# Kernel tuning notes

Hardware: AMD Instinct MI355X
Metric: run time of the kernel (lower is better)

Reference implementation:

```python
import jax, jax.numpy as jnp
import numpy as np

H = 16
D_MODEL = 1024
D_K = D_MODEL // H  # 64


def setup_inputs() -> dict:
    key = jax.random.key(0)
    ks = jax.random.split(key, 8)
    B, S = 8, 1024
    q = jax.random.normal(ks[0], (B, S, D_MODEL), dtype=jnp.float32)
    k = jax.random.normal(ks[1], (B, S, D_MODEL), dtype=jnp.float32)
    v = jax.random.normal(ks[2], (B, S, D_MODEL), dtype=jnp.float32)
    # xavier_normal for [h, d_model, d_k]: std = sqrt(2 / (d_model + d_k)) (fan over last two dims)
    std_p = float(np.sqrt(2.0 / (D_MODEL + D_K)))
    W_q = jax.random.normal(ks[3], (H, D_MODEL, D_K), dtype=jnp.float32) * std_p
    W_k = jax.random.normal(ks[4], (H, D_MODEL, D_K), dtype=jnp.float32) * std_p
    W_v = jax.random.normal(ks[5], (H, D_MODEL, D_K), dtype=jnp.float32) * std_p
    std_o = float(np.sqrt(2.0 / (H * D_K + D_MODEL)))
    W_o = jax.random.normal(ks[6], (D_MODEL, H * D_K), dtype=jnp.float32) * std_o  # torch Linear weight [out, in]
    b_o = jax.random.normal(ks[7], (D_MODEL,), dtype=jnp.float32) * 0.01
    return {"q": q, "k": k, "v": v, "W_q": W_q, "W_k": W_k, "W_v": W_v, "W_o": W_o, "b_o": b_o}


def reference(q, k, v, W_q, W_k, W_v, W_o, b_o):
    B, S, _ = q.shape
    # per-head projections: [h, b, s, d_k]
    qh = jnp.einsum('bsd,hdk->hbsk', q, W_q)
    kh = jnp.einsum('bsd,hdk->hbsk', k, W_k)
    vh = jnp.einsum('bsd,hdk->hbsk', v, W_v)
    scale = 1.0 / jnp.sqrt(jnp.asarray(D_K, dtype=q.dtype))
    scores = jnp.einsum('hbsk,hbtk->hbst', qh, kh) * scale  # [h,b,s,s]
    attn = jax.nn.softmax(scores, axis=-1)
    c = jnp.einsum('hbst,hbtk->hbsk', attn, vh)  # [h,b,s,d_k]
    # torch code splits the stacked (h*b) batch and concats on feature dim:
    # head index becomes the OUTER factor of the feature dim -> [b,s,h*d_k]
    c = jnp.transpose(c, (1, 2, 0, 3)).reshape(B, S, H * D_K)
    out = c @ W_o.T + b_o
    return out
```

## Files before the change

### kernel.cpp

```cpp
#include <hip/hip_runtime.h>
#include <hip/hip_bf16.h>

typedef __bf16 bf16_t;
typedef __attribute__((ext_vector_type(8))) __bf16 bf16x8;
typedef __attribute__((ext_vector_type(4))) float f32x4;

#define MFMA(a, b, c) __builtin_amdgcn_mfma_f32_16x16x32_bf16(a, b, c, 0, 0, 0)

__device__ inline void gload_lds16(const bf16_t* g, bf16_t* l) {
  __builtin_amdgcn_global_load_lds(
      (const __attribute__((address_space(1))) void*)g,
      (__attribute__((address_space(3))) void*)l, 16, 0, 0);
}

__global__ void fill_sentinel(float* out, int n, float val) {
  int i = blockIdx.x * blockDim.x + threadIdx.x;
  if (i < n) out[i] = val;
}

__global__ void transpose_w(const float* __restrict__ Wq, const float* __restrict__ Wk,
                            const float* __restrict__ Wv, bf16_t* __restrict__ Wt) {
  int gid = blockIdx.x * blockDim.x + threadIdx.x;
  int e = gid * 8;
  int m = e >> 20;
  int rem = e & 1048575;
  int n = rem >> 10;
  int d0 = rem & 1023;
  const float* W = (m == 0) ? Wq : (m == 1) ? Wk : Wv;
  int h = n >> 6, kk = n & 63;
  union { bf16_t h8[8]; uint4 u; } tmp;
#pragma unroll
  for (int j = 0; j < 8; ++j)
    tmp.h8[j] = (bf16_t)W[((size_t)(h * 1024 + d0 + j)) * 64 + kk];
  *(uint4*)(Wt + e) = tmp.u;
}

__global__ void cvt_bf16(const float* __restrict__ in, bf16_t* __restrict__ out) {
  size_t i = (size_t)(blockIdx.x * blockDim.x + threadIdx.x) * 8;
  f32x4 a = *(const f32x4*)(in + i);
  f32x4 b = *(const f32x4*)(in + i + 4);
  bf16x8 r;
  r[0] = (bf16_t)a[0]; r[1] = (bf16_t)a[1]; r[2] = (bf16_t)a[2]; r[3] = (bf16_t)a[3];
  r[4] = (bf16_t)b[0]; r[5] = (bf16_t)b[1]; r[6] = (bf16_t)b[2]; r[7] = (bf16_t)b[3];
  *(bf16x8*)(out + i) = r;
}

template <int MODE>
__global__ void gemm_bt(const bf16_t* __restrict__ A, const bf16_t* __restrict__ Bt,
                        const float* __restrict__ bias, void* __restrict__ out_,
                        int M, int N, int K, float scale) {
  __shared__ bf16_t sA[128 * 32];
  __shared__ bf16_t sB[128 * 32];
  const int t = threadIdx.x;
  const int w = t >> 6, l = t & 63;
  const int lq = l >> 4, ll = l & 15;
  const int m0 = blockIdx.x * 128, n0 = blockIdx.y * 128;
  const int wr = (w >> 1) * 64, wc = (w & 1) * 64;
  const int srow = l >> 2;
  const int scol = (l & 3) * 8;
  f32x4 acc[4][4] = {};
  for (int k0 = 0; k0 < K; k0 += 32) {
    __syncthreads();
#pragma unroll
    for (int c = 0; c < 2; ++c) {
      int ch = w * 2 + c;
      int row = ch * 16 + srow;
      gload_lds16(A  + (size_t)(m0 + row) * K + k0 + scol, sA + ch * 512);
      gload_lds16(Bt + (size_t)(n0 + row) * K + k0 + scol, sB + ch * 512);
    }
    __syncthreads();
    bf16x8 af[4], bfr[4];
#pragma unroll
    for (int i = 0; i < 4; ++i) {
      af[i]  = *(const bf16x8*)(sA + (wr + i * 16 + ll) * 32 + lq * 8);
      bfr[i] = *(const bf16x8*)(sB + (wc + i * 16 + ll) * 32 + lq * 8);
    }
#pragma unroll
    for (int mi = 0; mi < 4; ++mi)
#pragma unroll
      for (int ni = 0; ni < 4; ++ni)
        acc[mi][ni] = MFMA(af[mi], bfr[ni], acc[mi][ni]);
  }
#pragma unroll
  for (int mi = 0; mi < 4; ++mi)
#pragma unroll
    for (int ni = 0; ni < 4; ++ni)
#pragma unroll
      for (int r = 0; r < 4; ++r) {
        int row = m0 + wr + mi * 16 + lq * 4 + r;
        int col = n0 + wc + ni * 16 + ll;
        float v = acc[mi][ni][r];
        if (MODE == 2) {
          ((float*)out_)[(size_t)row * N + col] = v + bias[col];
        } else {
          int h = col >> 6, kk = col & 63, b = row >> 10, s = row & 1023;
          size_t idx;
          if (MODE == 0)
            idx = ((size_t)((h * 8 + b) * 1024 + s)) * 64 + kk;
          else
            idx = ((size_t)((h * 8 + b) * 64 + kk)) * 1024 + s;
          ((bf16_t*)out_)[idx] = (bf16_t)(v * scale);
        }
      }
}

__global__ void attn_kernel(const bf16_t* __restrict__ qh, const bf16_t* __restrict__ kh,
                            const bf16_t* __restrict__ vt, bf16_t* __restrict__ c) {
  constexpr int QP = 72, KP = 72, PP = 72;
  __shared__ bf16_t sQ[64 * QP];
  __shared__ bf16_t sK[64 * KP];
  __shared__ bf16_t sP[4][16 * PP];
  const int t = threadIdx.x;
  const int w = t >> 6, l = t & 63;
  const int lq = l >> 4, ll = l & 15;
  const int orig = blockIdx.x + (blockIdx.y << 4);
  const int wg = (orig & 7) * 256 + (orig >> 3);
  const int q0 = (wg & 15) * 64;
  const int hb = wg >> 4;
  const int h = hb >> 3, b = hb & 7;
  const size_t base = (size_t)hb * 65536;
  const bf16_t* Q = qh + base + (size_t)q0 * 64;
  const bf16_t* K = kh + base;
  const bf16_t* V = vt + base;
#pragma unroll
  for (int r = 0; r < 2; ++r) {
    int e = (r * 256 + t) * 8;
    int row = e >> 6, col = e & 63;
    *(uint4*)(sQ + row * QP + col) = *(const uint4*)(Q + e);
  }
  float mrow[4], lrow[4];
  f32x4 o[4] = {};
#pragma unroll
  for (int r = 0; r < 4; ++r) { mrow[r] = -1e30f; lrow[r] = 0.f; }

  for (int kt = 0; kt < 1024; kt += 64) {
    __syncthreads();
#pragma unroll
    for (int r = 0; r < 2; ++r) {
      int e = (r * 256 + t) * 8;
      int row = e >> 6, col = e & 63;
      *(uint4*)(sK + row * KP + col) = *(const uint4*)(K + (size_t)kt * 64 + e);
    }
    __syncthreads();
    f32x4 sacc[4] = {};
    bf16x8 aq[2];
#pragma unroll
    for (int ks = 0; ks < 2; ++ks)
      aq[ks] = *(const bf16x8*)(sQ + (w * 16 + ll) * QP + ks * 32 + lq * 8);
#pragma unroll
    for (int ni = 0; ni < 4; ++ni)
#pragma unroll
      for (int ks = 0; ks < 2; ++ks) {
        bf16x8 bk = *(const bf16x8*)(sK + (ni * 16 + ll) * KP + ks * 32 + lq * 8);
        sacc[ni] = MFMA(aq[ks], bk, sacc[ni]);
      }
    float rmax[4] = {-1e30f, -1e30f, -1e30f, -1e30f};
#pragma unroll
    for (int ni = 0; ni < 4; ++ni)
#pragma unroll
      for (int r = 0; r < 4; ++r)
        rmax[r] = fmaxf(rmax[r], sacc[ni][r]);
    bool ok = true;
#pragma unroll
    for (int r = 0; r < 4; ++r)
      ok = ok && (rmax[r] <= mrow[r] + 8.0f);
    if (!__all(ok)) {
#pragma unroll
      for (int off = 1; off < 16; off <<= 1)
#pragma unroll
        for (int r = 0; r < 4; ++r)
          rmax[r] = fmaxf(rmax[r], __shfl_xor(rmax[r], off));
#pragma unroll
      for (int r = 0; r < 4; ++r) {
        float mnew = fmaxf(mrow[r], rmax[r]);
        float alpha = __expf(mrow[r] - mnew);
        mrow[r] = mnew;
        lrow[r] *= alpha;
#pragma unroll
        for (int ni = 0; ni < 4; ++ni)
          o[ni][r] *= alpha;
      }
    }
#pragma unroll
    for (int ni = 0; ni < 4; ++ni)
#pragma unroll
      for (int r = 0; r < 4; ++r) {
        float p = __expf(sacc[ni][r] - mrow[r]);
        sacc[ni][r] = p;
        lrow[r] += p;
      }
    bf16_t* Pw = sP[w];
#pragma unroll
    for (int ni = 0; ni < 4; ++ni)
#pragma unroll
      for (int r = 0; r < 4; ++r)
        Pw[(lq * 4 + r) * PP + ni * 16 + ll] = (bf16_t)sacc[ni][r];
    asm volatile("s_waitcnt lgkmcnt(0)" ::: "memory");
#pragma unroll
    for (int ks = 0; ks < 2; ++ks) {
      bf16x8 ap = *(const bf16x8*)(Pw + ll * PP + ks * 32 + lq * 8);
#pragma unroll
      for (int ni = 0; ni < 4; ++ni) {
        bf16x8 bv = *(const bf16x8*)(V + (size_t)(ni * 16 + ll) * 1024 + kt + ks * 32 + lq * 8);
        o[ni] = MFMA(ap, bv, o[ni]);
      }
    }
  }
#pragma unroll
  for (int off = 1; off < 16; off <<= 1)
#pragma unroll
    for (int r = 0; r < 4; ++r)
      lrow[r] += __shfl_xor(lrow[r], off);
#pragma unroll
  for (int ni = 0; ni < 4; ++ni)
#pragma unroll
    for (int r = 0; r < 4; ++r) {
      int s = q0 + w * 16 + lq * 4 + r;
      int dk = ni * 16 + ll;
      float val = o[ni][r] / lrow[r];
      c[((size_t)(b * 1024 + s)) * 1024 + h * 64 + dk] = (bf16_t)val;
    }
}

extern "C" void kernel_launch(void* const* d_in, const int* in_sizes, int n_in,
                              void* d_out, int out_size, void* d_ws, size_t ws_size,
                              hipStream_t stream) {
  float* out = (float*)d_out;
  int nblk_out = (out_size + 255) / 256;
  if (n_in != 8) {
    fill_sentinel<<<nblk_out, 256, 0, stream>>>(out, out_size, 600.0f + 10.0f * n_in);
    return;
  }
  const int expect[8] = {8388608, 8388608, 8388608, 1048576,
                         1048576, 1048576, 1048576, 1024};
  for (int i = 0; i < 8; ++i)
    if (in_sizes[i] != expect[i]) {
      fill_sentinel<<<nblk_out, 256, 0, stream>>>(out, out_size, 500.0f + 10.0f * i);
      return;
    }

  bf16_t* ws   = (bf16_t*)d_ws;
  bf16_t* qhb  = ws;
  bf16_t* khb  = ws + 8388608;
  bf16_t* vtb  = ws + 16777216;
  bf16_t* Wt   = ws + 25165824;
  bf16_t* cbuf = ws + 25165824;
  bf16_t* Wob  = ws;
  if (ws_size < 67108864ull) {
    fill_sentinel<<<nblk_out, 256, 0, stream>>>(out, out_size, 400.0f);
    return;
  }

  const float* q  = (const float*)d_in[0];
  const float* k  = (const float*)d_in[1];
  const float* v  = (const float*)d_in[2];
  const float* Wq = (const float*)d_in[3];
  const float* Wk = (const float*)d_in[4];
  const float* Wv = (const float*)d_in[5];
  const float* Wo = (const float*)d_in[6];
  const float* bo = (const float*)d_in[7];

  bf16_t* qb = (bf16_t*)d_out;
  bf16_t* kb = (bf16_t*)d_out + 8388608;
  bf16_t* vb = (bf16_t*)d_out;

  transpose_w<<<1536, 256, 0, stream>>>(Wq, Wk, Wv, Wt);
  cvt_bf16<<<4096, 256, 0, stream>>>(q, qb);
  cvt_bf16<<<4096, 256, 0, stream>>>(k, kb);
  dim3 gg(64, 8);
  gemm_bt<0><<<gg, 256, 0, stream>>>(qb, Wt,           nullptr, qhb, 8192, 1024, 1024, 0.125f);
  gemm_bt<0><<<gg, 256, 0, stream>>>(kb, Wt + 1048576, nullptr, khb, 8192, 1024, 1024, 1.0f);
  cvt_bf16<<<4096, 256, 0, stream>>>(v, vb);
  gemm_bt<1><<<gg, 256, 0, stream>>>(vb, Wt + 2097152, nullptr, vtb, 8192, 1024, 1024, 1.0f);
  attn_kernel<<<dim3(16, 128), 256, 0, stream>>>(qhb, khb, vtb, cbuf);
  cvt_bf16<<<512, 256, 0, stream>>>(Wo, Wob);
  gemm_bt<2><<<gg, 256, 0, stream>>>(cbuf, Wob, bo, out, 8192, 1024, 1024, 1.0f);
}
```

Before: 429.2 us.

## Double-buffer K tiles via registers and prefetch V in attention loop

The attention kernel now loads Q fragments straight into registers instead of staging them in shared memory. K tiles are double-buffered: the next tile is fetched into registers at the start of each iteration and written to the alternate LDS buffer at the end, so one barrier per iteration replaces two. V fragments are issued early, before the QK MFMAs, to hide global latency. The cost is higher register pressure, which may lower occupancy.

Result: slower. 451.9 us (+5.3%).

```diff
diff --git a/kernel.cpp b/kernel.cpp
--- a/kernel.cpp
+++ b/kernel.cpp
@@ -106,9 +106,8 @@
 
 __global__ void attn_kernel(const bf16_t* __restrict__ qh, const bf16_t* __restrict__ kh,
                             const bf16_t* __restrict__ vt, bf16_t* __restrict__ c) {
-  constexpr int QP = 72, KP = 72, PP = 72;
-  __shared__ bf16_t sQ[64 * QP];
-  __shared__ bf16_t sK[64 * KP];
+  constexpr int KP = 72, PP = 72;
+  __shared__ bf16_t sK[2][64 * KP];
   __shared__ bf16_t sP[4][16 * PP];
   const int t = threadIdx.x;
   const int w = t >> 6, l = t & 63;
@@ -122,36 +121,52 @@
   const bf16_t* Q = qh + base + (size_t)q0 * 64;
   const bf16_t* K = kh + base;
   const bf16_t* V = vt + base;
+
+  bf16x8 aq[2];
+#pragma unroll
+  for (int ks = 0; ks < 2; ++ks)
+    aq[ks] = *(const bf16x8*)(Q + (w * 16 + ll) * 64 + ks * 32 + lq * 8);
+
+  uint4 kreg[2];
+#pragma unroll
+  for (int r = 0; r < 2; ++r) {
+    int e = (r * 256 + t) * 8;
+    kreg[r] = *(const uint4*)(K + e);
+  }
 #pragma unroll
   for (int r = 0; r < 2; ++r) {
     int e = (r * 256 + t) * 8;
     int row = e >> 6, col = e & 63;
-    *(uint4*)(sQ + row * QP + col) = *(const uint4*)(Q + e);
-  }
+    *(uint4*)(sK[0] + row * KP + col) = kreg[r];
+  }
+  __syncthreads();
+
   float mrow[4], lrow[4];
   f32x4 o[4] = {};
 #pragma unroll
   for (int r = 0; r < 4; ++r) { mrow[r] = -1e30f; lrow[r] = 0.f; }
 
-  for (int kt = 0; kt < 1024; kt += 64) {
-    __syncthreads();
-#pragma unroll
-    for (int r = 0; r < 2; ++r) {
-      int e = (r * 256 + t) * 8;
-      int row = e >> 6, col = e & 63;
-      *(uint4*)(sK + row * KP + col) = *(const uint4*)(K + (size_t)kt * 64 + e);
-    }
-    __syncthreads();
+  int cur = 0;
+  for (int kt = 0; kt < 1024; kt += 64, cur ^= 1) {
+    if (kt + 64 < 1024) {
+#pragma unroll
+      for (int r = 0; r < 2; ++r) {
+        int e = (r * 256 + t) * 8;
+        kreg[r] = *(const uint4*)(K + (size_t)(kt + 64) * 64 + e);
+      }
+    }
+    bf16x8 bv[2][4];
+#pragma unroll
+    for (int ks = 0; ks < 2; ++ks)
+#pragma unroll
+      for (int ni = 0; ni < 4; ++ni)
+        bv[ks][ni] = *(const bf16x8*)(V + (size_t)(ni * 16 + ll) * 1024 + kt + ks * 32 + lq * 8);
     f32x4 sacc[4] = {};
-    bf16x8 aq[2];
-#pragma unroll
-    for (int ks = 0; ks < 2; ++ks)
-      aq[ks] = *(const bf16x8*)(sQ + (w * 16 + ll) * QP + ks * 32 + lq * 8);
 #pragma unroll
     for (int ni = 0; ni < 4; ++ni)
 #pragma unroll
       for (int ks = 0; ks < 2; ++ks) {
-        bf16x8 bk = *(const bf16x8*)(sK + (ni * 16 + ll) * KP + ks * 32 + lq * 8);
+        bf16x8 bk = *(const bf16x8*)(sK[cur] + (ni * 16 + ll) * KP + ks * 32 + lq * 8);
         sacc[ni] = MFMA(aq[ks], bk, sacc[ni]);
       }
     float rmax[4] = {-1e30f, -1e30f, -1e30f, -1e30f};
@@ -200,11 +215,18 @@
     for (int ks = 0; ks < 2; ++ks) {
       bf16x8 ap = *(const bf16x8*)(Pw + ll * PP + ks * 32 + lq * 8);
 #pragma unroll
-      for (int ni = 0; ni < 4; ++ni) {
-        bf16x8 bv = *(const bf16x8*)(V + (size_t)(ni * 16 + ll) * 1024 + kt + ks * 32 + lq * 8);
-        o[ni] = MFMA(ap, bv, o[ni]);
-      }
-    }
+      for (int ni = 0; ni < 4; ++ni)
+        o[ni] = MFMA(ap, bv[ks][ni], o[ni]);
+    }
+    if (kt + 64 < 1024) {
+#pragma unroll
+      for (int r = 0; r < 2; ++r) {
+        int e = (r * 256 + t) * 8;
+        int row = e >> 6, col = e & 63;
+        *(uint4*)(sK[cur ^ 1] + row * KP + col) = kreg[r];
+      }
+    }
+    __syncthreads();
   }
 #pragma unroll
   for (int off = 1; off < 16; off <<= 1)
```

## Double-buffer K tiles, hoist V loads, and transpose the score MFMA layout

Applied to the files above, without the earlier changes.

The attention kernel now double-buffers K in shared memory and prefetches the next K tile into registers while computing on the current one, so each tile needs one barrier instead of two. V fragments are loaded from global at the top of each iteration so their latency overlaps the QK^T MFMAs. The Q fragments are read directly from global into registers, and the score MFMA operands are swapped so each lane owns one query row. That turns the per-row max and sum into scalars with fewer shuffles and lets P be written to shared memory as packed 4-element stores. It also adds s_setprio around the MFMA blocks, at the cost of more registers and some cross-lane shuffles when rescaling.

Measured after the change: 410.0 us. 1.05x faster.

```diff
diff --git a/kernel.cpp b/kernel.cpp
--- a/kernel.cpp
+++ b/kernel.cpp
@@ -106,9 +106,8 @@
 
 __global__ void attn_kernel(const bf16_t* __restrict__ qh, const bf16_t* __restrict__ kh,
                             const bf16_t* __restrict__ vt, bf16_t* __restrict__ c) {
-  constexpr int QP = 72, KP = 72, PP = 72;
-  __shared__ bf16_t sQ[64 * QP];
-  __shared__ bf16_t sK[64 * KP];
+  constexpr int KP = 72, PP = 72;
+  __shared__ bf16_t sK[2][64 * KP];
   __shared__ bf16_t sP[4][16 * PP];
   const int t = threadIdx.x;
   const int w = t >> 6, l = t & 63;
@@ -122,104 +121,121 @@
   const bf16_t* Q = qh + base + (size_t)q0 * 64;
   const bf16_t* K = kh + base;
   const bf16_t* V = vt + base;
-#pragma unroll
-  for (int r = 0; r < 2; ++r) {
-    int e = (r * 256 + t) * 8;
-    int row = e >> 6, col = e & 63;
-    *(uint4*)(sQ + row * QP + col) = *(const uint4*)(Q + e);
-  }
-  float mrow[4], lrow[4];
+
+  bf16x8 aq0 = *(const bf16x8*)(Q + (w * 16 + ll) * 64 + 0 * 32 + lq * 8);
+  bf16x8 aq1 = *(const bf16x8*)(Q + (w * 16 + ll) * 64 + 1 * 32 + lq * 8);
+
+  {
+    int e0 = t * 8, e1 = (256 + t) * 8;
+    uint4 ka = *(const uint4*)(K + e0);
+    uint4 kb = *(const uint4*)(K + e1);
+    *(uint4*)(sK[0] + (e0 >> 6) * KP + (e0 & 63)) = ka;
+    *(uint4*)(sK[0] + (e1 >> 6) * KP + (e1 & 63)) = kb;
+  }
+  __syncthreads();
+
+  float mrow = -1e30f, lrow = 0.f;
   f32x4 o[4] = {};
-#pragma unroll
-  for (int r = 0; r < 4; ++r) { mrow[r] = -1e30f; lrow[r] = 0.f; }
-
-  for (int kt = 0; kt < 1024; kt += 64) {
+  bf16_t* Pw = sP[w];
+
+  int cur = 0;
+  for (int kt = 0; kt < 1024; kt += 64, cur ^= 1) {
+    uint4 kr0, kr1;
+    if (kt < 960) {
+      kr0 = *(const uint4*)(K + (size_t)(kt + 64) * 64 + t * 8);
+      kr1 = *(const uint4*)(K + (size_t)(kt + 64) * 64 + (256 + t) * 8);
+    }
+    const bf16_t* Vb = V + (size_t)ll * 1024 + kt + lq * 8;
+    bf16x8 bv00 = *(const bf16x8*)(Vb + 0 * 16384 + 0);
+    bf16x8 bv01 = *(const bf16x8*)(Vb + 1 * 16384 + 0);
+    bf16x8 bv02 = *(const bf16x8*)(Vb + 2 * 16384 + 0);
+    bf16x8 bv03 = *(const bf16x8*)(Vb + 3 * 16384 + 0);
+    bf16x8 bv10 = *(const bf16x8*)(Vb + 0 * 16384 + 32);
+    bf16x8 bv11 = *(const bf16x8*)(Vb + 1 * 16384 + 32);
+    bf16x8 bv12 = *(const bf16x8*)(Vb + 2 * 16384 + 32);
+    bf16x8 bv13 = *(const bf16x8*)(Vb + 3 * 16384 + 32);
+
+    f32x4 sacc[4] = {};
+    __builtin_amdgcn_s_setprio(1);
+#pragma unroll
+    for (int ni = 0; ni < 4; ++ni) {
+      bf16x8 bk0 = *(const bf16x8*)(sK[cur] + (ni * 16 + ll) * KP + 0 * 32 + lq * 8);
+      bf16x8 bk1 = *(const bf16x8*)(sK[cur] + (ni * 16 + ll) * KP + 1 * 32 + lq * 8);
+      sacc[ni] = MFMA(bk0, aq0, sacc[ni]);
+      sacc[ni] = MFMA(bk1, aq1, sacc[ni]);
+    }
+    __builtin_amdgcn_s_setprio(0);
+    float rmax = -1e30f;
+#pragma unroll
+    for (int ni = 0; ni < 4; ++ni)
+#pragma unroll
+      for (int r = 0; r < 4; ++r)
+        rmax = fmaxf(rmax, sacc[ni][r]);
+    if (!__all(rmax <= mrow + 8.0f)) {
+      rmax = fmaxf(rmax, __shfl_xor(rmax, 16));
+      rmax = fmaxf(rmax, __shfl_xor(rmax, 32));
+      float mnew = fmaxf(mrow, rmax);
+      float alpha = __expf(mrow - mnew);
+      mrow = mnew;
+      lrow *= alpha;
+#pragma unroll
+      for (int r = 0; r < 4; ++r) {
+        float ar = __shfl(alpha, lq * 4 + r, 16);
+#pragma unroll
+        for (int ni = 0; ni < 4; ++ni)
+          o[ni][r] *= ar;
+      }
+    }
+#pragma unroll
+    for (int ni = 0; ni < 4; ++ni)
+#pragma unroll
+      for (int r = 0; r < 4; ++r) {
+        float p = __expf(sacc[ni][r] - mrow);
+        sacc[ni][r] = p;
+        lrow += p;
+      }
+#pragma unroll
+    for (int ni = 0; ni < 4; ++ni) {
+      union { bf16_t h4[4]; uint2 u; } pk;
+      pk.h4[0] = (bf16_t)sacc[ni][0];
+      pk.h4[1] = (bf16_t)sacc[ni][1];
+      pk.h4[2] = (bf16_t)sacc[ni][2];
+      pk.h4[3] = (bf16_t)sacc[ni][3];
+      *(uint2*)(Pw + ll * PP + ni * 16 + lq * 4) = pk.u;
+    }
+    asm volatile("s_waitcnt lgkmcnt(0)" ::: "memory");
+    __builtin_amdgcn_sched_barrier(0);
+    bf16x8 ap0 = *(const bf16x8*)(Pw + ll * PP + 0 * 32 + lq * 8);
+    bf16x8 ap1 = *(const bf16x8*)(Pw + ll * PP + 1 * 32 + lq * 8);
+    __builtin_amdgcn_s_setprio(1);
+    o[0] = MFMA(ap0, bv00, o[0]);
+    o[1] = MFMA(ap0, bv01, o[1]);
+    o[2] = MFMA(ap0, bv02, o[2]);
+    o[3] = MFMA(ap0, bv03, o[3]);
+    o[0] = MFMA(ap1, bv10, o[0]);
+    o[1] = MFMA(ap1, bv11, o[1]);
+    o[2] = MFMA(ap1, bv12, o[2]);
+    o[3] = MFMA(ap1, bv13, o[3]);
+    __builtin_amdgcn_s_setprio(0);
+    if (kt < 960) {
+      int e0 = t * 8, e1 = (256 + t) * 8;
+      *(uint4*)(sK[cur ^ 1] + (e0 >> 6) * KP + (e0 & 63)) = kr0;
+      *(uint4*)(sK[cur ^ 1] + (e1 >> 6) * KP + (e1 & 63)) = kr1;
+    }
     __syncthreads();
-#pragma unroll
-    for (int r = 0; r < 2; ++r) {
-      int e = (r * 256 + t) * 8;
-      int row = e >> 6, col = e & 63;
-      *(uint4*)(sK + row * KP + col) = *(const uint4*)(K + (size_t)kt * 64 + e);
-    }
-    __syncthreads();
-    f32x4 sacc[4] = {};
-    bf16x8 aq[2];
-#pragma unroll
-    for (int ks = 0; ks < 2; ++ks)
-      aq[ks] = *(const bf16x8*)(sQ + (w * 16 + ll) * QP + ks * 32 + lq * 8);
-#pragma unroll
-    for (int ni = 0; ni < 4; ++ni)
-#pragma unroll
-      for (int ks = 0; ks < 2; ++ks) {
-        bf16x8 bk = *(const bf16x8*)(sK + (ni * 16 + ll) * KP + ks * 32 + lq * 8);
-        sacc[ni] = MFMA(aq[ks], bk, sacc[ni]);
-      }
-    float rmax[4] = {-1e30f, -1e30f, -1e30f, -1e30f};
-#pragma unroll
-    for (int ni = 0; ni < 4; ++ni)
-#pragma unroll
-      for (int r = 0; r < 4; ++r)
-        rmax[r] = fmaxf(rmax[r], sacc[ni][r]);
-    bool ok = true;
-#pragma unroll
-    for (int r = 0; r < 4; ++r)
-      ok = ok && (rmax[r] <= mrow[r] + 8.0f);
-    if (!__all(ok)) {
-#pragma unroll
-      for (int off = 1; off < 16; off <<= 1)
-#pragma unroll
-        for (int r = 0; r < 4; ++r)
-          rmax[r] = fmaxf(rmax[r], __shfl_xor(rmax[r], off));
-#pragma unroll
-      for (int r = 0; r < 4; ++r) {
-        float mnew = fmaxf(mrow[r], rmax[r]);
-        float alpha = __expf(mrow[r] - mnew);
-        mrow[r] = mnew;
-        lrow[r] *= alpha;
-#pragma unroll
-        for (int ni = 0; ni < 4; ++ni)
-          o[ni][r] *= alpha;
-      }
-    }
-#pragma unroll
-    for (int ni = 0; ni < 4; ++ni)
-#pragma unroll
-      for (int r = 0; r < 4; ++r) {
-        float p = __expf(sacc[ni][r] - mrow[r]);
-        sacc[ni][r] = p;
-        lrow[r] += p;
-      }
-    bf16_t* Pw = sP[w];
-#pragma unroll
-    for (int ni = 0; ni < 4; ++ni)
-#pragma unroll
-      for (int r = 0; r < 4; ++r)
-        Pw[(lq * 4 + r) * PP + ni * 16 + ll] = (bf16_t)sacc[ni][r];
-    asm volatile("s_waitcnt lgkmcnt(0)" ::: "memory");
-#pragma unroll
-    for (int ks = 0; ks < 2; ++ks) {
-      bf16x8 ap = *(const bf16x8*)(Pw + ll * PP + ks * 32 + lq * 8);
-#pragma unroll
-      for (int ni = 0; ni < 4; ++ni) {
-        bf16x8 bv = *(const bf16x8*)(V + (size_t)(ni * 16 + ll) * 1024 + kt + ks * 32 + lq * 8);
-        o[ni] = MFMA(ap, bv, o[ni]);
-      }
-    }
-  }
-#pragma unroll
-  for (int off = 1; off < 16; off <<= 1)
-#pragma unroll
-    for (int r = 0; r < 4; ++r)
-      lrow[r] += __shfl_xor(lrow[r], off);
-#pragma unroll
-  for (int ni = 0; ni < 4; ++ni)
-#pragma unroll
-    for (int r = 0; r < 4; ++r) {
-      int s = q0 + w * 16 + lq * 4 + r;
+  }
+  lrow += __shfl_xor(lrow, 16);
+  lrow += __shfl_xor(lrow, 32);
+#pragma unroll
+  for (int r = 0; r < 4; ++r) {
+    float lr = __shfl(lrow, lq * 4 + r, 16);
+    int s = q0 + w * 16 + lq * 4 + r;
+#pragma unroll
+    for (int ni = 0; ni < 4; ++ni) {
       int dk = ni * 16 + ll;
-      float val = o[ni][r] / lrow[r];
-      c[((size_t)(b * 1024 + s)) * 1024 + h * 64 + dk] = (bf16_t)val;
-    }
+      c[((size_t)(b * 1024 + s)) * 1024 + h * 64 + dk] = (bf16_t)(o[ni][r] / lr);
+    }
+  }
 }
 
 extern "C" void kernel_launch(void* const* d_in, const int* in_sizes, int n_in,
```
